# Optimization experiments

Hardware: AMD Instinct MI355X
Metric: run time of the kernel (lower is better)

The kernel has to match this reference:

```python
import jax, jax.numpy as jnp
import numpy as np

HIDDEN = 256
HEADS = 8
N = 4096

def setup_inputs() -> dict:
    key = jax.random.key(0)
    ks = jax.random.split(key, 6)
    s = 1.0 / np.sqrt(HIDDEN)
    return {
        "inputs": jax.random.normal(ks[0], (N, HIDDEN), dtype=jnp.float32),
        "Wq": jax.random.uniform(ks[1], (HIDDEN, HIDDEN), jnp.float32, -s, s),
        "Wk": jax.random.uniform(ks[2], (HIDDEN, HIDDEN), jnp.float32, -s, s),
        "Wv": jax.random.uniform(ks[3], (HIDDEN, HIDDEN), jnp.float32, -s, s),
        "Wf": jax.random.uniform(ks[4], (HIDDEN, HIDDEN), jnp.float32, -s, s),
        "bf": jax.random.uniform(ks[5], (HIDDEN,), jnp.float32, -s, s),
    }

def reference(inputs, Wq, Wk, Wv, Wf, bf):
    d_head = HIDDEN // HEADS
    # q/k/v projections (torch Linear: x @ W.T), then split heads: [h, n, d]
    def split_heads(x):
        return x.reshape(N, HEADS, d_head).transpose(1, 0, 2)
    q = split_heads(inputs @ Wq.T)
    k = split_heads(inputs @ Wk.T)
    v = split_heads(inputs @ Wv.T)
    # tanh-gated attention: no softmax normalizer (dropout p=0 -> identity)
    score = jnp.tanh(jnp.einsum('hnd,hmd->hnm', q, k))  # [h, N, N]
    att = jnp.einsum('hnm,hmd->hnd', score, v)            # [h, N, d]
    att = att.transpose(1, 0, 2).reshape(N, HIDDEN)
    att_hidden = jax.nn.relu(att @ Wf.T + bf)
    return (inputs, att_hidden)
```

## Files before the change

### kernel.cpp

```cpp
#include <hip/hip_runtime.h>
#include <math.h>

#define N_TOK 4096
#define HID 256
#define D_HEAD 32
#define N_HEADS 8
#define NSEG 4

typedef __bf16 bf16x8 __attribute__((ext_vector_type(8)));
typedef float f32x4 __attribute__((ext_vector_type(4)));
typedef unsigned short u16x8 __attribute__((ext_vector_type(8)));

static __device__ __forceinline__ unsigned short bf16_bits(float f) {
  __bf16 h = (__bf16)f;
  return __builtin_bit_cast(unsigned short, h);
}
static __device__ __forceinline__ float bf16_val(unsigned short u) {
  return (float)__builtin_bit_cast(__bf16, u);
}

static __device__ __forceinline__ float r_of(float x2) {
  float e = __builtin_amdgcn_exp2f(x2);
  return __builtin_amdgcn_rcpf(1.0f + e);
}

static __device__ __forceinline__ bf16x8 pack8(float4 a, float4 b) {
  bf16x8 v;
  v[0] = (__bf16)a.x; v[1] = (__bf16)a.y; v[2] = (__bf16)a.z; v[3] = (__bf16)a.w;
  v[4] = (__bf16)b.x; v[5] = (__bf16)b.y; v[6] = (__bf16)b.z; v[7] = (__bf16)b.w;
  return v;
}

__global__ __launch_bounds__(256) void prep(
    const float* __restrict__ X,
    const float* __restrict__ Wq, const float* __restrict__ Wk,
    const float* __restrict__ Wv,
    float* __restrict__ out0, unsigned short* __restrict__ Xb,
    unsigned short* __restrict__ Wqb, unsigned short* __restrict__ Wkb,
    unsigned short* __restrict__ Wvb)
{
  const int b = blockIdx.x;
  const int tid = threadIdx.x;
  if (b < 512) {
    const size_t base = ((size_t)b * 256 + tid) * 8;
    float4 a = *(const float4*)(X + base);
    float4 c = *(const float4*)(X + base + 4);
    *(float4*)(out0 + base) = a;
    *(float4*)(out0 + base + 4) = c;
    *(bf16x8*)(Xb + base) = pack8(a, c);
  } else {
    const int r = b - 512;
    const int w = r >> 5;
    const float* W = (w == 0) ? Wq : (w == 1) ? Wk : Wv;
    unsigned short* O = (w == 0) ? Wqb : (w == 1) ? Wkb : Wvb;
    const size_t base = ((size_t)(r & 31) * 256 + tid) * 8;
    float4 a = *(const float4*)(W + base);
    float4 c = *(const float4*)(W + base + 4);
    *(bf16x8*)(O + base) = pack8(a, c);
  }
}

__global__ __launch_bounds__(256, 4) void proj_qkv(
    const unsigned short* __restrict__ Xb,
    const unsigned short* __restrict__ Wqb,
    const unsigned short* __restrict__ Wkb,
    const unsigned short* __restrict__ Wvb,
    unsigned short* __restrict__ Qws, unsigned short* __restrict__ Kws,
    unsigned short* __restrict__ Vws)
{
  const int lane = threadIdx.x & 63;
  const int wid  = threadIdx.x >> 6;
  const int lr = lane & 15, lg = lane >> 4;
  const int mb = blockIdx.x * 64 + (wid >> 1) * 32;
  const int ob = blockIdx.y * 64 + (wid & 1) * 32;
  const int z  = blockIdx.z;
  const unsigned short* W = (z == 0) ? Wqb : (z == 1) ? Wkb : Wvb;

  f32x4 acc[2][2];
#pragma unroll
  for (int i = 0; i < 2; ++i)
#pragma unroll
    for (int j = 0; j < 2; ++j) acc[i][j] = (f32x4){0.f, 0.f, 0.f, 0.f};

#pragma unroll 2
  for (int kb = 0; kb < HID; kb += 32) {
    bf16x8 af[2], bfr[2];
#pragma unroll
    for (int mi = 0; mi < 2; ++mi)
      af[mi] = *(const bf16x8*)(Xb + (size_t)(mb + mi * 16 + lr) * HID + kb + lg * 8);
#pragma unroll
    for (int oi = 0; oi < 2; ++oi)
      bfr[oi] = *(const bf16x8*)(W + (size_t)(ob + oi * 16 + lr) * HID + kb + lg * 8);
#pragma unroll
    for (int mi = 0; mi < 2; ++mi)
#pragma unroll
      for (int oi = 0; oi < 2; ++oi)
        acc[mi][oi] = __builtin_amdgcn_mfma_f32_16x16x32_bf16(
            af[mi], bfr[oi], acc[mi][oi], 0, 0, 0);
  }

  const float qscale = (z == 0) ? 2.885390081777927f : 1.0f;

#pragma unroll
  for (int mi = 0; mi < 2; ++mi)
#pragma unroll
    for (int oi = 0; oi < 2; ++oi)
#pragma unroll
      for (int r = 0; r < 4; ++r) {
        const int n = mb + mi * 16 + lg * 4 + r;
        const int o = ob + oi * 16 + lr;
        const unsigned short bits = bf16_bits(acc[mi][oi][r] * qscale);
        const int h = o >> 5, d = o & 31;
        if (z < 2) {
          unsigned short* OUT = (z == 0) ? Qws : Kws;
          OUT[((size_t)h * N_TOK + n) * D_HEAD + d] = bits;
        } else {
          const int rr = n & 31;
          const int slot = (rr < 16) ? ((rr >> 2) * 8 + (rr & 3))
                                     : (((rr - 16) >> 2) * 8 + 4 + (rr & 3));
          Vws[(size_t)h * (N_TOK * D_HEAD) + (size_t)(n >> 5) * 1024 + d * 32 + slot] = bits;
        }
      }
}

struct Frags { bf16x8 k[2][2], v[2][2]; };

static __device__ __forceinline__ Frags load_phase(
    const unsigned short* __restrict__ Kh,
    const unsigned short* __restrict__ Vh, size_t base)
{
  Frags f;
#pragma unroll
  for (int s = 0; s < 2; ++s)
#pragma unroll
    for (int h = 0; h < 2; ++h) {
      f.k[s][h] = *(const bf16x8*)(Kh + base + s * 1024 + h * 512);
      f.v[s][h] = *(const bf16x8*)(Vh + base + s * 1024 + h * 512);
    }
  return f;
}

__global__ __launch_bounds__(256, 2) void attn_kernel(
    const unsigned short* __restrict__ Qws,
    const unsigned short* __restrict__ Kws,
    const unsigned short* __restrict__ Vws,
    unsigned short* __restrict__ part)
{
  __shared__ float tanh_tab[4640];
  __shared__ __align__(16) float lds_t[4][16 * 36];

  for (int i = threadIdx.x; i < 4609; i += 256)
    tanh_tab[i] = tanhf((float)(i - 2304) * (1.0f / 512.0f));
  __syncthreads();

  const int lane = threadIdx.x & 63;
  const int wid  = threadIdx.x >> 6;
  const int b    = blockIdx.x;
  const int head = b & 7;
  const int inner = b >> 3;
  const int qsplit = inner >> 2;
  const int seg    = inner & 3;
  const int qbase  = qsplit * 256 + wid * 64;
  const int kstart = seg * (N_TOK / NSEG);
  const int NT = (N_TOK / NSEG) / 64;

  const unsigned short* Qh = Qws + (size_t)head * N_TOK * D_HEAD;
  const unsigned short* Kh = Kws + (size_t)head * N_TOK * D_HEAD;
  const unsigned short* Vh = Vws + (size_t)head * N_TOK * D_HEAD;

  const int lr = lane & 15, lg = lane >> 4;

  bf16x8 qf[4];
#pragma unroll
  for (int m = 0; m < 4; ++m)
    qf[m] = *(const bf16x8*)(Qh + (size_t)(qbase + m * 16 + lr) * 32 + lg * 8);

  bf16x8 onesf;
#pragma unroll
  for (int j = 0; j < 8; ++j) onesf[j] = (__bf16)1.0f;

  const f32x4 z4 = {0.f, 0.f, 0.f, 0.f};
  f32x4 alo[4], ahi[4];
#pragma unroll
  for (int m = 0; m < 4; ++m) { alo[m] = z4; ahi[m] = z4; }
  f32x4 clo = z4, chi = z4;

  const size_t fb = (size_t)kstart * 32 + lr * 32 + lg * 8;

  #define LUT_TANH(x2) ({                                                 \
    float _t = __builtin_fmaf((x2), 177.4456782f, 2304.5f);               \
    _t = __builtin_amdgcn_fmed3f(_t, 0.5f, 4608.5f);                      \
    tanh_tab[(int)_t]; })

  Frags fA = load_phase(Kh, Vh, fb);

  for (int t = 0; t < NT; t += 2) {
    Frags fB = load_phase(Kh, Vh, fb + (size_t)(t + 1) * 2048);
    __builtin_amdgcn_sched_barrier(0);

#pragma unroll
    for (int s = 0; s < 2; ++s) {
#pragma unroll
      for (int m = 0; m < 4; ++m) {
        f32x4 s0 = __builtin_amdgcn_mfma_f32_16x16x32_bf16(fA.k[s][0], qf[m], z4, 0, 0, 0);
        f32x4 s1 = __builtin_amdgcn_mfma_f32_16x16x32_bf16(fA.k[s][1], qf[m], z4, 0, 0, 0);
        bf16x8 pf;
        if (m < 2) {
#pragma unroll
          for (int r = 0; r < 4; ++r) pf[r]     = (__bf16)r_of(s0[r]);
#pragma unroll
          for (int r = 0; r < 4; ++r) pf[4 + r] = (__bf16)r_of(s1[r]);
        } else {
#pragma unroll
          for (int r = 0; r < 4; ++r) pf[r]     = (__bf16)LUT_TANH(s0[r]);
#pragma unroll
          for (int r = 0; r < 4; ++r) pf[4 + r] = (__bf16)LUT_TANH(s1[r]);
        }
        alo[m] = __builtin_amdgcn_mfma_f32_16x16x32_bf16(fA.v[s][0], pf, alo[m], 0, 0, 0);
        ahi[m] = __builtin_amdgcn_mfma_f32_16x16x32_bf16(fA.v[s][1], pf, ahi[m], 0, 0, 0);
      }
      clo = __builtin_amdgcn_mfma_f32_16x16x32_bf16(fA.v[s][0], onesf, clo, 0, 0, 0);
      chi = __builtin_amdgcn_mfma_f32_16x16x32_bf16(fA.v[s][1], onesf, chi, 0, 0, 0);
    }

    if (t + 2 < NT) fA = load_phase(Kh, Vh, fb + (size_t)(t + 2) * 2048);
    __builtin_amdgcn_sched_barrier(0);

#pragma unroll
    for (int s = 0; s < 2; ++s) {
#pragma unroll
      for (int m = 0; m < 4; ++m) {
        f32x4 s0 = __builtin_amdgcn_mfma_f32_16x16x32_bf16(fB.k[s][0], qf[m], z4, 0, 0, 0);
        f32x4 s1 = __builtin_amdgcn_mfma_f32_16x16x32_bf16(fB.k[s][1], qf[m], z4, 0, 0, 0);
        bf16x8 pf;
        if (m < 2) {
#pragma unroll
          for (int r = 0; r < 4; ++r) pf[r]     = (__bf16)r_of(s0[r]);
#pragma unroll
          for (int r = 0; r < 4; ++r) pf[4 + r] = (__bf16)r_of(s1[r]);
        } else {
#pragma unroll
          for (int r = 0; r < 4; ++r) pf[r]     = (__bf16)LUT_TANH(s0[r]);
#pragma unroll
          for (int r = 0; r < 4; ++r) pf[4 + r] = (__bf16)LUT_TANH(s1[r]);
        }
        alo[m] = __builtin_amdgcn_mfma_f32_16x16x32_bf16(fB.v[s][0], pf, alo[m], 0, 0, 0);
        ahi[m] = __builtin_amdgcn_mfma_f32_16x16x32_bf16(fB.v[s][1], pf, ahi[m], 0, 0, 0);
      }
      clo = __builtin_amdgcn_mfma_f32_16x16x32_bf16(fB.v[s][0], onesf, clo, 0, 0, 0);
      chi = __builtin_amdgcn_mfma_f32_16x16x32_bf16(fB.v[s][1], onesf, chi, 0, 0, 0);
    }
  }
  #undef LUT_TANH

  float* L = &lds_t[wid][0];
  const int qloc = lane >> 2, chunk = lane & 3;
#pragma unroll
  for (int m = 0; m < 4; ++m) {
#pragma unroll
    for (int r = 0; r < 4; ++r) {
      if (m < 2) {
        L[lr * 36 + lg * 4 + r]      = __builtin_fmaf(alo[m][r], -2.0f, clo[r]);
        L[lr * 36 + 16 + lg * 4 + r] = __builtin_fmaf(ahi[m][r], -2.0f, chi[r]);
      } else {
        L[lr * 36 + lg * 4 + r]      = alo[m][r];
        L[lr * 36 + 16 + lg * 4 + r] = ahi[m][r];
      }
    }
    f32x4 va = *(const f32x4*)&L[qloc * 36 + chunk * 4];
    f32x4 vb = *(const f32x4*)&L[qloc * 36 + 16 + chunk * 4];
    ushort4 oa, ob;
    oa.x = bf16_bits(va[0]); oa.y = bf16_bits(va[1]);
    oa.z = bf16_bits(va[2]); oa.w = bf16_bits(va[3]);
    ob.x = bf16_bits(vb[0]); ob.y = bf16_bits(vb[1]);
    ob.z = bf16_bits(vb[2]); ob.w = bf16_bits(vb[3]);
    unsigned short* dst = part + ((size_t)seg * N_TOK + qbase + m * 16 + qloc) * HID
                        + head * 32 + chunk * 4;
    *(ushort4*)dst        = oa;
    *(ushort4*)(dst + 16) = ob;
  }
}

__global__ __launch_bounds__(256, 2) void final_proj(
    const unsigned short* __restrict__ part, const float* __restrict__ Wf,
    const float* __restrict__ bias, float* __restrict__ out)
{
  __shared__ __align__(16) unsigned short Alds[16][264];

  const int tid  = threadIdx.x;
  const int lane = tid & 63;
  const int wid  = tid >> 6;
  const int lr = lane & 15, lg = lane >> 4;
  const int mb = blockIdx.x * 16;
  const int cb = blockIdx.y * 128;

  {
    const int row = tid >> 4, c0 = (tid & 15) * 16;
    const size_t off = (size_t)(mb + row) * HID + c0;
    float s[16];
#pragma unroll
    for (int j = 0; j < 16; ++j) s[j] = 0.f;
#pragma unroll
    for (int sg = 0; sg < NSEG; ++sg) {
      u16x8 u0 = *(const u16x8*)(part + (size_t)sg * N_TOK * HID + off);
      u16x8 u1 = *(const u16x8*)(part + (size_t)sg * N_TOK * HID + off + 8);
#pragma unroll
      for (int j = 0; j < 8; ++j) { s[j] += bf16_val(u0[j]); s[8 + j] += bf16_val(u1[j]); }
    }
    bf16x8 o0, o1;
#pragma unroll
    for (int j = 0; j < 8; ++j) { o0[j] = (__bf16)s[j]; o1[j] = (__bf16)s[8 + j]; }
    *(bf16x8*)&Alds[row][c0]     = o0;
    *(bf16x8*)&Alds[row][c0 + 8] = o1;
  }
  __syncthreads();

  f32x4 acc[2];
  acc[0] = (f32x4){0.f, 0.f, 0.f, 0.f};
  acc[1] = (f32x4){0.f, 0.f, 0.f, 0.f};

#pragma unroll 2
  for (int kb = 0; kb < HID; kb += 32) {
    bf16x8 af = *(const bf16x8*)&Alds[lr][kb + lg * 8];
#pragma unroll
    for (int y = 0; y < 2; ++y) {
      const int ob = cb + y * 64 + wid * 16;
      const float* p = Wf + (size_t)(ob + lr) * HID + kb + lg * 8;
      bf16x8 bfr = pack8(*(const float4*)p, *(const float4*)(p + 4));
      acc[y] = __builtin_amdgcn_mfma_f32_16x16x32_bf16(af, bfr, acc[y], 0, 0, 0);
    }
  }

#pragma unroll
  for (int y = 0; y < 2; ++y)
#pragma unroll
    for (int r = 0; r < 4; ++r) {
      const int n = mb + lg * 4 + r;
      const int o = cb + y * 64 + wid * 16 + lr;
      float v = acc[y][r] + bias[o];
      out[(size_t)n * HID + o] = fmaxf(v, 0.f);
    }
}

extern "C" void kernel_launch(void* const* d_in, const int* in_sizes, int n_in,
                              void* d_out, int out_size, void* d_ws, size_t ws_size,
                              hipStream_t stream)
{
  const float* X  = (const float*)d_in[0];
  const float* Wq = (const float*)d_in[1];
  const float* Wk = (const float*)d_in[2];
  const float* Wv = (const float*)d_in[3];
  const float* Wf = (const float*)d_in[4];
  const float* bf = (const float*)d_in[5];
  float* out = (float*)d_out;

  unsigned char* ws = (unsigned char*)d_ws;
  unsigned short* Qws  = (unsigned short*)(ws);
  unsigned short* Kws  = (unsigned short*)(ws + (2u << 20));
  unsigned short* Vws  = (unsigned short*)(ws + (4u << 20));
  unsigned short* PART = (unsigned short*)(ws + (6u << 20));
  unsigned short* Xb   = (unsigned short*)(ws + (6u << 20));
  unsigned short* Wqb  = (unsigned short*)(ws + (8u << 20));
  unsigned short* Wkb  = (unsigned short*)(ws + (8u << 20) + (128u << 10));
  unsigned short* Wvb  = (unsigned short*)(ws + (8u << 20) + (256u << 10));

  prep<<<dim3(608), 256, 0, stream>>>(X, Wq, Wk, Wv, out, Xb, Wqb, Wkb, Wvb);
  proj_qkv<<<dim3(64, 4, 3), 256, 0, stream>>>(Xb, Wqb, Wkb, Wvb, Qws, Kws, Vws);
  attn_kernel<<<dim3(8 * 16 * NSEG), 256, 0, stream>>>(Qws, Kws, Vws, PART);
  final_proj<<<dim3(256, 2), 256, 0, stream>>>(PART, Wf, bf, out + (size_t)N_TOK * HID);
}
```

Before: 71.90 us.

## Split attention waves by activation path and widen blocks to 512 threads

```diff
diff --git a/kernel.cpp b/kernel.cpp
--- a/kernel.cpp
+++ b/kernel.cpp
@@ -140,27 +140,28 @@
   return f;
 }
 
-__global__ __launch_bounds__(256, 2) void attn_kernel(
+__global__ __launch_bounds__(512, 1) void attn_kernel(
     const unsigned short* __restrict__ Qws,
     const unsigned short* __restrict__ Kws,
     const unsigned short* __restrict__ Vws,
     unsigned short* __restrict__ part)
 {
   __shared__ float tanh_tab[4640];
-  __shared__ __align__(16) float lds_t[4][16 * 36];
-
-  for (int i = threadIdx.x; i < 4609; i += 256)
+  __shared__ __align__(16) float lds_t[8][16 * 36];
+
+  for (int i = threadIdx.x; i < 4609; i += 512)
     tanh_tab[i] = tanhf((float)(i - 2304) * (1.0f / 512.0f));
   __syncthreads();
 
   const int lane = threadIdx.x & 63;
   const int wid  = threadIdx.x >> 6;
+  const int wpath = __builtin_amdgcn_readfirstlane(wid);
   const int b    = blockIdx.x;
   const int head = b & 7;
   const int inner = b >> 3;
   const int qsplit = inner >> 2;
   const int seg    = inner & 3;
-  const int qbase  = qsplit * 256 + wid * 64;
+  const int qbase  = qsplit * 256 + wid * 32;
   const int kstart = seg * (N_TOK / NSEG);
   const int NT = (N_TOK / NSEG) / 64;
 
@@ -170,20 +171,15 @@
 
   const int lr = lane & 15, lg = lane >> 4;
 
-  bf16x8 qf[4];
-#pragma unroll
-  for (int m = 0; m < 4; ++m)
+  bf16x8 qf[2];
+#pragma unroll
+  for (int m = 0; m < 2; ++m)
     qf[m] = *(const bf16x8*)(Qh + (size_t)(qbase + m * 16 + lr) * 32 + lg * 8);
 
-  bf16x8 onesf;
-#pragma unroll
-  for (int j = 0; j < 8; ++j) onesf[j] = (__bf16)1.0f;
-
   const f32x4 z4 = {0.f, 0.f, 0.f, 0.f};
-  f32x4 alo[4], ahi[4];
-#pragma unroll
-  for (int m = 0; m < 4; ++m) { alo[m] = z4; ahi[m] = z4; }
-  f32x4 clo = z4, chi = z4;
+  f32x4 alo[2], ahi[2];
+#pragma unroll
+  for (int m = 0; m < 2; ++m) { alo[m] = z4; ahi[m] = z4; }
 
   const size_t fb = (size_t)kstart * 32 + lr * 32 + lg * 8;
 
@@ -192,96 +188,137 @@
     _t = __builtin_amdgcn_fmed3f(_t, 0.5f, 4608.5f);                      \
     tanh_tab[(int)_t]; })
 
-  Frags fA = load_phase(Kh, Vh, fb);
-
-  for (int t = 0; t < NT; t += 2) {
-    Frags fB = load_phase(Kh, Vh, fb + (size_t)(t + 1) * 2048);
-    __builtin_amdgcn_sched_barrier(0);
-
-#pragma unroll
-    for (int s = 0; s < 2; ++s) {
-#pragma unroll
-      for (int m = 0; m < 4; ++m) {
-        f32x4 s0 = __builtin_amdgcn_mfma_f32_16x16x32_bf16(fA.k[s][0], qf[m], z4, 0, 0, 0);
-        f32x4 s1 = __builtin_amdgcn_mfma_f32_16x16x32_bf16(fA.k[s][1], qf[m], z4, 0, 0, 0);
-        bf16x8 pf;
-        if (m < 2) {
-#pragma unroll
-          for (int r = 0; r < 4; ++r) pf[r]     = (__bf16)r_of(s0[r]);
-#pragma unroll
-          for (int r = 0; r < 4; ++r) pf[4 + r] = (__bf16)r_of(s1[r]);
-        } else {
-#pragma unroll
-          for (int r = 0; r < 4; ++r) pf[r]     = (__bf16)LUT_TANH(s0[r]);
-#pragma unroll
-          for (int r = 0; r < 4; ++r) pf[4 + r] = (__bf16)LUT_TANH(s1[r]);
-        }
-        alo[m] = __builtin_amdgcn_mfma_f32_16x16x32_bf16(fA.v[s][0], pf, alo[m], 0, 0, 0);
-        ahi[m] = __builtin_amdgcn_mfma_f32_16x16x32_bf16(fA.v[s][1], pf, ahi[m], 0, 0, 0);
-      }
-      clo = __builtin_amdgcn_mfma_f32_16x16x32_bf16(fA.v[s][0], onesf, clo, 0, 0, 0);
-      chi = __builtin_amdgcn_mfma_f32_16x16x32_bf16(fA.v[s][1], onesf, chi, 0, 0, 0);
-    }
-
-    if (t + 2 < NT) fA = load_phase(Kh, Vh, fb + (size_t)(t + 2) * 2048);
-    __builtin_amdgcn_sched_barrier(0);
-
-#pragma unroll
-    for (int s = 0; s < 2; ++s) {
-#pragma unroll
-      for (int m = 0; m < 4; ++m) {
-        f32x4 s0 = __builtin_amdgcn_mfma_f32_16x16x32_bf16(fB.k[s][0], qf[m], z4, 0, 0, 0);
-        f32x4 s1 = __builtin_amdgcn_mfma_f32_16x16x32_bf16(fB.k[s][1], qf[m], z4, 0, 0, 0);
-        bf16x8 pf;
-        if (m < 2) {
-#pragma unroll
-          for (int r = 0; r < 4; ++r) pf[r]     = (__bf16)r_of(s0[r]);
-#pragma unroll
-          for (int r = 0; r < 4; ++r) pf[4 + r] = (__bf16)r_of(s1[r]);
-        } else {
-#pragma unroll
-          for (int r = 0; r < 4; ++r) pf[r]     = (__bf16)LUT_TANH(s0[r]);
-#pragma unroll
-          for (int r = 0; r < 4; ++r) pf[4 + r] = (__bf16)LUT_TANH(s1[r]);
-        }
-        alo[m] = __builtin_amdgcn_mfma_f32_16x16x32_bf16(fB.v[s][0], pf, alo[m], 0, 0, 0);
-        ahi[m] = __builtin_amdgcn_mfma_f32_16x16x32_bf16(fB.v[s][1], pf, ahi[m], 0, 0, 0);
-      }
-      clo = __builtin_amdgcn_mfma_f32_16x16x32_bf16(fB.v[s][0], onesf, clo, 0, 0, 0);
-      chi = __builtin_amdgcn_mfma_f32_16x16x32_bf16(fB.v[s][1], onesf, chi, 0, 0, 0);
-    }
-  }
-  #undef LUT_TANH
-
   float* L = &lds_t[wid][0];
   const int qloc = lane >> 2, chunk = lane & 3;
-#pragma unroll
-  for (int m = 0; m < 4; ++m) {
-#pragma unroll
-    for (int r = 0; r < 4; ++r) {
-      if (m < 2) {
+
+  if (wpath < 4) {
+    bf16x8 onesf;
+#pragma unroll
+    for (int j = 0; j < 8; ++j) onesf[j] = (__bf16)1.0f;
+    f32x4 clo = z4, chi = z4;
+
+    Frags fA = load_phase(Kh, Vh, fb);
+    for (int t = 0; t < NT; t += 2) {
+      Frags fB = load_phase(Kh, Vh, fb + (size_t)(t + 1) * 2048);
+      __builtin_amdgcn_sched_barrier(0);
+#pragma unroll
+      for (int s = 0; s < 2; ++s) {
+#pragma unroll
+        for (int m = 0; m < 2; ++m) {
+          f32x4 s0 = __builtin_amdgcn_mfma_f32_16x16x32_bf16(fA.k[s][0], qf[m], z4, 0, 0, 0);
+          f32x4 s1 = __builtin_amdgcn_mfma_f32_16x16x32_bf16(fA.k[s][1], qf[m], z4, 0, 0, 0);
+          bf16x8 pf;
+#pragma unroll
+          for (int r = 0; r < 4; ++r) pf[r]     = (__bf16)r_of(s0[r]);
+#pragma unroll
+          for (int r = 0; r < 4; ++r) pf[4 + r] = (__bf16)r_of(s1[r]);
+          alo[m] = __builtin_amdgcn_mfma_f32_16x16x32_bf16(fA.v[s][0], pf, alo[m], 0, 0, 0);
+          ahi[m] = __builtin_amdgcn_mfma_f32_16x16x32_bf16(fA.v[s][1], pf, ahi[m], 0, 0, 0);
+        }
+        clo = __builtin_amdgcn_mfma_f32_16x16x32_bf16(fA.v[s][0], onesf, clo, 0, 0, 0);
+        chi = __builtin_amdgcn_mfma_f32_16x16x32_bf16(fA.v[s][1], onesf, chi, 0, 0, 0);
+      }
+      if (t + 2 < NT) fA = load_phase(Kh, Vh, fb + (size_t)(t + 2) * 2048);
+      __builtin_amdgcn_sched_barrier(0);
+#pragma unroll
+      for (int s = 0; s < 2; ++s) {
+#pragma unroll
+        for (int m = 0; m < 2; ++m) {
+          f32x4 s0 = __builtin_amdgcn_mfma_f32_16x16x32_bf16(fB.k[s][0], qf[m], z4, 0, 0, 0);
+          f32x4 s1 = __builtin_amdgcn_mfma_f32_16x16x32_bf16(fB.k[s][1], qf[m], z4, 0, 0, 0);
+          bf16x8 pf;
+#pragma unroll
+          for (int r = 0; r < 4; ++r) pf[r]     = (__bf16)r_of(s0[r]);
+#pragma unroll
+          for (int r = 0; r < 4; ++r) pf[4 + r] = (__bf16)r_of(s1[r]);
+          alo[m] = __builtin_amdgcn_mfma_f32_16x16x32_bf16(fB.v[s][0], pf, alo[m], 0, 0, 0);
+          ahi[m] = __builtin_amdgcn_mfma_f32_16x16x32_bf16(fB.v[s][1], pf, ahi[m], 0, 0, 0);
+        }
+        clo = __builtin_amdgcn_mfma_f32_16x16x32_bf16(fB.v[s][0], onesf, clo, 0, 0, 0);
+        chi = __builtin_amdgcn_mfma_f32_16x16x32_bf16(fB.v[s][1], onesf, chi, 0, 0, 0);
+      }
+    }
+
+#pragma unroll
+    for (int m = 0; m < 2; ++m) {
+#pragma unroll
+      for (int r = 0; r < 4; ++r) {
         L[lr * 36 + lg * 4 + r]      = __builtin_fmaf(alo[m][r], -2.0f, clo[r]);
         L[lr * 36 + 16 + lg * 4 + r] = __builtin_fmaf(ahi[m][r], -2.0f, chi[r]);
-      } else {
+      }
+      f32x4 va = *(const f32x4*)&L[qloc * 36 + chunk * 4];
+      f32x4 vb = *(const f32x4*)&L[qloc * 36 + 16 + chunk * 4];
+      ushort4 oa, ob;
+      oa.x = bf16_bits(va[0]); oa.y = bf16_bits(va[1]);
+      oa.z = bf16_bits(va[2]); oa.w = bf16_bits(va[3]);
+      ob.x = bf16_bits(vb[0]); ob.y = bf16_bits(vb[1]);
+      ob.z = bf16_bits(vb[2]); ob.w = bf16_bits(vb[3]);
+      unsigned short* dst = part + ((size_t)seg * N_TOK + qbase + m * 16 + qloc) * HID
+                          + head * 32 + chunk * 4;
+      *(ushort4*)dst        = oa;
+      *(ushort4*)(dst + 16) = ob;
+    }
+  } else {
+    Frags fA = load_phase(Kh, Vh, fb);
+    for (int t = 0; t < NT; t += 2) {
+      Frags fB = load_phase(Kh, Vh, fb + (size_t)(t + 1) * 2048);
+      __builtin_amdgcn_sched_barrier(0);
+#pragma unroll
+      for (int s = 0; s < 2; ++s)
+#pragma unroll
+        for (int m = 0; m < 2; ++m) {
+          f32x4 s0 = __builtin_amdgcn_mfma_f32_16x16x32_bf16(fA.k[s][0], qf[m], z4, 0, 0, 0);
+          f32x4 s1 = __builtin_amdgcn_mfma_f32_16x16x32_bf16(fA.k[s][1], qf[m], z4, 0, 0, 0);
+          bf16x8 pf;
+#pragma unroll
+          for (int r = 0; r < 4; ++r) pf[r]     = (__bf16)LUT_TANH(s0[r]);
+#pragma unroll
+          for (int r = 0; r < 4; ++r) pf[4 + r] = (__bf16)LUT_TANH(s1[r]);
+          alo[m] = __builtin_amdgcn_mfma_f32_16x16x32_bf16(fA.v[s][0], pf, alo[m], 0, 0, 0);
+          ahi[m] = __builtin_amdgcn_mfma_f32_16x16x32_bf16(fA.v[s][1], pf, ahi[m], 0, 0, 0);
+        }
+      if (t + 2 < NT) fA = load_phase(Kh, Vh, fb + (size_t)(t + 2) * 2048);
+      __builtin_amdgcn_sched_barrier(0);
+#pragma unroll
+      for (int s = 0; s < 2; ++s)
+#pragma unroll
+        for (int m = 0; m < 2; ++m) {
+          f32x4 s0 = __builtin_amdgcn_mfma_f32_16x16x32_bf16(fB.k[s][0], qf[m], z4, 0, 0, 0);
+          f32x4 s1 = __builtin_amdgcn_mfma_f32_16x16x32_bf16(fB.k[s][1], qf[m], z4, 0, 0, 0);
+          bf16x8 pf;
+#pragma unroll
+          for (int r = 0; r < 4; ++r) pf[r]     = (__bf16)LUT_TANH(s0[r]);
+#pragma unroll
+          for (int r = 0; r < 4; ++r) pf[4 + r] = (__bf16)LUT_TANH(s1[r]);
+          alo[m] = __builtin_amdgcn_mfma_f32_16x16x32_bf16(fB.v[s][0], pf, alo[m], 0, 0, 0);
+          ahi[m] = __builtin_amdgcn_mfma_f32_16x16x32_bf16(fB.v[s][1], pf, ahi[m], 0, 0, 0);
+        }
+    }
+
+#pragma unroll
+    for (int m = 0; m < 2; ++m) {
+#pragma unroll
+      for (int r = 0; r < 4; ++r) {
         L[lr * 36 + lg * 4 + r]      = alo[m][r];
         L[lr * 36 + 16 + lg * 4 + r] = ahi[m][r];
       }
-    }
-    f32x4 va = *(const f32x4*)&L[qloc * 36 + chunk * 4];
-    f32x4 vb = *(const f32x4*)&L[qloc * 36 + 16 + chunk * 4];
-    ushort4 oa, ob;
-    oa.x = bf16_bits(va[0]); oa.y = bf16_bits(va[1]);
-    oa.z = bf16_bits(va[2]); oa.w = bf16_bits(va[3]);
-    ob.x = bf16_bits(vb[0]); ob.y = bf16_bits(vb[1]);
-    ob.z = bf16_bits(vb[2]); ob.w = bf16_bits(vb[3]);
-    unsigned short* dst = part + ((size_t)seg * N_TOK + qbase + m * 16 + qloc) * HID
-                        + head * 32 + chunk * 4;
-    *(ushort4*)dst        = oa;
-    *(ushort4*)(dst + 16) = ob;
+      f32x4 va = *(const f32x4*)&L[qloc * 36 + chunk * 4];
+      f32x4 vb = *(const f32x4*)&L[qloc * 36 + 16 + chunk * 4];
+      ushort4 oa, ob;
+      oa.x = bf16_bits(va[0]); oa.y = bf16_bits(va[1]);
+      oa.z = bf16_bits(va[2]); oa.w = bf16_bits(va[3]);
+      ob.x = bf16_bits(vb[0]); ob.y = bf16_bits(vb[1]);
+      ob.z = bf16_bits(vb[2]); ob.w = bf16_bits(vb[3]);
+      unsigned short* dst = part + ((size_t)seg * N_TOK + qbase + m * 16 + qloc) * HID
+                          + head * 32 + chunk * 4;
+      *(ushort4*)dst        = oa;
+      *(ushort4*)(dst + 16) = ob;
+    }
   }
-}
-
-__global__ __launch_bounds__(256, 2) void final_proj(
+  #undef LUT_TANH
+}
+
+__global__ __launch_bounds__(512, 2) void final_proj(
     const unsigned short* __restrict__ part, const float* __restrict__ Wf,
     const float* __restrict__ bias, float* __restrict__ out)
 {
@@ -292,26 +329,23 @@
   const int wid  = tid >> 6;
   const int lr = lane & 15, lg = lane >> 4;
   const int mb = blockIdx.x * 16;
-  const int cb = blockIdx.y * 128;
 
   {
-    const int row = tid >> 4, c0 = (tid & 15) * 16;
+    const int row = tid >> 5, c0 = (tid & 31) * 8;
     const size_t off = (size_t)(mb + row) * HID + c0;
-    float s[16];
-#pragma unroll
-    for (int j = 0; j < 16; ++j) s[j] = 0.f;
+    float s[8];
+#pragma unroll
+    for (int j = 0; j < 8; ++j) s[j] = 0.f;
 #pragma unroll
     for (int sg = 0; sg < NSEG; ++sg) {
-      u16x8 u0 = *(const u16x8*)(part + (size_t)sg * N_TOK * HID + off);
-      u16x8 u1 = *(const u16x8*)(part + (size_t)sg * N_TOK * HID + off + 8);
-#pragma unroll
-      for (int j = 0; j < 8; ++j) { s[j] += bf16_val(u0[j]); s[8 + j] += bf16_val(u1[j]); }
-    }
-    bf16x8 o0, o1;
-#pragma unroll
-    for (int j = 0; j < 8; ++j) { o0[j] = (__bf16)s[j]; o1[j] = (__bf16)s[8 + j]; }
-    *(bf16x8*)&Alds[row][c0]     = o0;
-    *(bf16x8*)&Alds[row][c0 + 8] = o1;
+      u16x8 u = *(const u16x8*)(part + (size_t)sg * N_TOK * HID + off);
+#pragma unroll
+      for (int j = 0; j < 8; ++j) s[j] += bf16_val(u[j]);
+    }
+    bf16x8 o8;
+#pragma unroll
+    for (int j = 0; j < 8; ++j) o8[j] = (__bf16)s[j];
+    *(bf16x8*)&Alds[row][c0] = o8;
   }
   __syncthreads();
 
@@ -324,7 +358,7 @@
     bf16x8 af = *(const bf16x8*)&Alds[lr][kb + lg * 8];
 #pragma unroll
     for (int y = 0; y < 2; ++y) {
-      const int ob = cb + y * 64 + wid * 16;
+      const int ob = wid * 32 + y * 16;
       const float* p = Wf + (size_t)(ob + lr) * HID + kb + lg * 8;
       bf16x8 bfr = pack8(*(const float4*)p, *(const float4*)(p + 4));
       acc[y] = __builtin_amdgcn_mfma_f32_16x16x32_bf16(af, bfr, acc[y], 0, 0, 0);
@@ -336,7 +370,7 @@
 #pragma unroll
     for (int r = 0; r < 4; ++r) {
       const int n = mb + lg * 4 + r;
-      const int o = cb + y * 64 + wid * 16 + lr;
+      const int o = wid * 32 + y * 16 + lr;
       float v = acc[y][r] + bias[o];
       out[(size_t)n * HID + o] = fmaxf(v, 0.f);
     }
@@ -366,6 +400,6 @@
 
   prep<<<dim3(608), 256, 0, stream>>>(X, Wq, Wk, Wv, out, Xb, Wqb, Wkb, Wvb);
   proj_qkv<<<dim3(64, 4, 3), 256, 0, stream>>>(Xb, Wqb, Wkb, Wvb, Qws, Kws, Vws);
-  attn_kernel<<<dim3(8 * 16 * NSEG), 256, 0, stream>>>(Qws, Kws, Vws, PART);
-  final_proj<<<dim3(256, 2), 256, 0, stream>>>(PART, Wf, bf, out + (size_t)N_TOK * HID);
-}
+  attn_kernel<<<dim3(8 * 16 * NSEG), 512, 0, stream>>>(Qws, Kws, Vws, PART);
+  final_proj<<<dim3(256), 512, 0, stream>>>(PART, Wf, bf, out + (size_t)N_TOK * HID);
+}
```

Result: slower. 74.67 us (+3.8%).
